# Kernel tuning notes

Measured on AMD Instinct MI355X. Metric: run time of the kernel, lower is better.

Reference implementation:

```python
import jax, jax.numpy as jnp
import numpy as np

R_RAYS = 65536
S_PER_RAY = 128
N_TOTAL = R_RAYS * S_PER_RAY


def setup_inputs() -> dict:
    key = jax.random.key(0)
    k1, k2, k3, k4 = jax.random.split(key, 4)
    sigmas = jax.random.uniform(k1, (N_TOTAL,), dtype=jnp.float32) * 2.0  # densities >= 0
    rgbs = jax.random.uniform(k2, (N_TOTAL, 3), dtype=jnp.float32)
    deltas = jax.random.uniform(k3, (N_TOTAL,), dtype=jnp.float32) * 0.01 + 1e-3
    ts = jax.random.uniform(k4, (N_TOTAL,), dtype=jnp.float32) * 6.0 + 0.1
    ray_idx = jnp.arange(R_RAYS, dtype=jnp.int32)
    rays_a = jnp.stack([ray_idx, ray_idx * S_PER_RAY,
                        jnp.full((R_RAYS,), S_PER_RAY, dtype=jnp.int32)], axis=1)
    return {"sigmas": sigmas, "rgbs": rgbs, "deltas": deltas, "ts": ts,
            "rays_a": rays_a, "T_threshold": 1e-4}


def reference(sigmas, rgbs, deltas, ts, rays_a, T_threshold):
    R = rays_a.shape[0]
    N = sigmas.shape[0]
    S_max = int(jnp.max(rays_a[:, 2]))  # max samples per ray (concrete)

    offs = jnp.arange(S_max, dtype=rays_a.dtype)
    valid = offs[None, :] < rays_a[:, 2, None]              # [R, S] prefix mask
    idx = jnp.where(valid, rays_a[:, 1, None] + offs[None, :], N - 1)  # [R, S]

    a = 1.0 - jnp.exp(-sigmas[idx] * deltas[idx])           # [R, S] alphas

    # Sequential transmittance recurrence with early-exit (T set to 0 once below threshold)
    def step(T, xs):
        a_s, v_s = xs                                        # [R], [R]
        alive = (T > T_threshold) & v_s
        w = jnp.where(alive, a_s * T, 0.0)
        T = jnp.where(alive, T * (1.0 - a_s), 0.0)
        return T, (w, alive)

    T0 = jnp.ones((R,), sigmas.dtype)
    _, (wT, aliveT) = jax.lax.scan(step, T0, (a.T, valid.T))
    w = wT.T                                                 # [R, S] weights
    alive = aliveT.T

    op_n = jnp.sum(w, axis=1)                                # [R]
    dep_n = jnp.sum(w * ts[idx], axis=1)                     # [R]
    rgb_n = jnp.einsum('rs,rsc->rc', w, rgbs[idx])           # [R, 3]
    cnt_n = jnp.sum(alive, axis=1).astype(jnp.int32)

    ridx = rays_a[:, 0]
    opacity = jnp.zeros((R,), w.dtype).at[ridx].add(op_n)
    depth = jnp.zeros((R,), w.dtype).at[ridx].add(dep_n)
    rgb = jnp.zeros((R, 3), w.dtype).at[ridx].add(rgb_n)
    total_samples = jnp.zeros((R,), jnp.int32).at[ridx].add(cnt_n)
    # invalid slots were mapped to index N-1 with w=0, so .add is safe
    ws = jnp.zeros((N,), w.dtype).at[idx.reshape(-1)].add(w.reshape(-1))

    return total_samples.sum(), opacity, depth, rgb, ws
```

## Files before the change

### kernel.cpp

```cpp
#include <hip/hip_runtime.h>


#define BW 4

typedef float f4a __attribute__((ext_vector_type(4), aligned(4)));

template<int CTRL, int RM, unsigned OLD>
__device__ __forceinline__ float dpp_f(float v) {
    return __int_as_float(__builtin_amdgcn_update_dpp(
        (int)OLD, __float_as_int(v), CTRL, RM, 0xF, false));
}

__device__ __forceinline__ float seg_sum32_hi(float v) {
    v += dpp_f<0x111, 0xF, 0u>(v);
    v += dpp_f<0x112, 0xF, 0u>(v);
    v += dpp_f<0x114, 0xF, 0u>(v);
    v += dpp_f<0x118, 0xF, 0u>(v);
    v += dpp_f<0x142, 0xA, 0u>(v);
    return v;
}

struct Ld { float4 sg, dt, tt, c0, c1, c2; };

__global__ __launch_bounds__(256) void vr_main(
    const float* __restrict__ sigmas, const float* __restrict__ rgbs,
    const float* __restrict__ deltas, const float* __restrict__ ts,
    const int* __restrict__ rays_a, const float* __restrict__ thr_p,
    float* __restrict__ out, float* __restrict__ blk_ws,
    int R, int use_ws, int spec_ok)
{
    __shared__ float bsum[BW];

    const int wib  = (int)(threadIdx.x >> 6);
    const int wid  = (int)blockIdx.x * BW + wib;
    const int lane = (int)(threadIdx.x & 63);
    const int half = lane >> 5;
    const int sl   = lane & 31;
    const int ray  = 2 * wid + half;
    const bool inR = ray < R;
    const float thr = thr_p[0];

    const int p_start = ray << 7;
    Ld d;
    if (spec_ok && inR) {
        d.sg = *(const float4*)(sigmas + p_start + 4 * sl);
        d.dt = *(const float4*)(deltas + p_start + 4 * sl);
        d.tt = *(const float4*)(ts     + p_start + 4 * sl);
        const float* rg = rgbs + 3 * ((size_t)p_start + 4 * sl);
        d.c0 = *(const float4*)(rg + 0);
        d.c1 = *(const float4*)(rg + 4);
        d.c2 = *(const float4*)(rg + 8);
    }

    int ridx = 0, start = 0, count = 0;
    if (inR) {
        ridx  = rays_a[3 * ray + 0];
        start = rays_a[3 * ray + 1];
        count = rays_a[3 * ray + 2];
    }
    const bool match = spec_ok && inR && (start == p_start) && (count == 128);
    const bool fastw = __all(match);

    if (!fastw) {
        float sg[4], dt[4], tt[4], rr[4], gg[4], bb[4];
        #pragma unroll
        for (int i = 0; i < 4; ++i) {
            const int s = 4 * sl + i;
            const bool vi = inR && (s < count);
            sg[i] = dt[i] = tt[i] = rr[i] = gg[i] = bb[i] = 0.f;
            if (vi) {
                sg[i] = sigmas[start + s];
                dt[i] = deltas[start + s];
                tt[i] = ts[start + s];
                const float* rg = rgbs + 3 * ((size_t)start + s);
                rr[i] = rg[0]; gg[i] = rg[1]; bb[i] = rg[2];
            }
        }
        d.sg = make_float4(sg[0], sg[1], sg[2], sg[3]);
        d.dt = make_float4(dt[0], dt[1], dt[2], dt[3]);
        d.tt = make_float4(tt[0], tt[1], tt[2], tt[3]);
        d.c0 = make_float4(rr[0], gg[0], bb[0], rr[1]);
        d.c1 = make_float4(gg[1], bb[1], rr[2], gg[2]);
        d.c2 = make_float4(bb[2], rr[3], gg[3], bb[3]);
    }

    float fe[4] = { __expf(-d.sg.x * d.dt.x), __expf(-d.sg.y * d.dt.y),
                    __expf(-d.sg.z * d.dt.z), __expf(-d.sg.w * d.dt.w) };
    bool v[4];
    #pragma unroll
    for (int i = 0; i < 4; ++i) v[i] = inR && (4 * sl + i) < count;

    const float fprod = (fe[0] * fe[1]) * (fe[2] * fe[3]);
    float inc = fprod;
    inc *= dpp_f<0x111, 0xF, 0x3f800000u>(inc);
    inc *= dpp_f<0x112, 0xF, 0x3f800000u>(inc);
    inc *= dpp_f<0x114, 0xF, 0x3f800000u>(inc);
    inc *= dpp_f<0x118, 0xF, 0x3f800000u>(inc);
    inc *= dpp_f<0x142, 0xA, 0x3f800000u>(inc);

    float ex = dpp_f<0x138, 0xF, 0x3f800000u>(inc);
    float T = (sl == 0) ? 1.f : ex;

    float w[4];
    float cnt = 0.f;
    #pragma unroll
    for (int i = 0; i < 4; ++i) {
        const bool alive = v[i] && (T > thr);
        const float Tn = T * fe[i];
        w[i] = alive ? (T - Tn) : 0.f;
        cnt += alive ? 1.f : 0.f;
        T = Tn;
    }

    float* wsp = out + 1 + 5 * (size_t)R + (size_t)start + 4 * sl;
    if (fastw) {
        f4a wv; wv.x = w[0]; wv.y = w[1]; wv.z = w[2]; wv.w = w[3];
        *(f4a*)wsp = wv;
    } else {
        #pragma unroll
        for (int i = 0; i < 4; ++i) if (v[i]) wsp[i] = w[i];
    }

    float op  = (w[0] + w[1]) + (w[2] + w[3]);
    float dep = fmaf(w[0], d.tt.x, fmaf(w[1], d.tt.y, fmaf(w[2], d.tt.z, w[3] * d.tt.w)));
    float cr  = fmaf(w[0], d.c0.x, fmaf(w[1], d.c0.w, fmaf(w[2], d.c1.z, w[3] * d.c2.y)));
    float cg  = fmaf(w[0], d.c0.y, fmaf(w[1], d.c1.x, fmaf(w[2], d.c1.w, w[3] * d.c2.z)));
    float cb  = fmaf(w[0], d.c0.z, fmaf(w[1], d.c1.y, fmaf(w[2], d.c2.x, w[3] * d.c2.w)));

    op  = seg_sum32_hi(op);
    dep = seg_sum32_hi(dep);
    cr  = seg_sum32_hi(cr);
    cg  = seg_sum32_hi(cg);
    cb  = seg_sum32_hi(cb);
    cnt = seg_sum32_hi(cnt);

    if (sl == 31 && inR) {
        out[1 + ridx]                 = op;
        out[1 + R + ridx]             = dep;
        out[1 + 2 * R + 3 * ridx + 0] = cr;
        out[1 + 2 * R + 3 * ridx + 1] = cg;
        out[1 + 2 * R + 3 * ridx + 2] = cb;
    }

    const float cw =
        __int_as_float(__builtin_amdgcn_readlane(__float_as_int(cnt), 31)) +
        __int_as_float(__builtin_amdgcn_readlane(__float_as_int(cnt), 63));
    if (lane == 0) bsum[wib] = cw;
    __syncthreads();
    if (threadIdx.x == 0) {
        const float t = (bsum[0] + bsum[1]) + (bsum[2] + bsum[3]);
        if (use_ws) blk_ws[blockIdx.x] = t;
        else        atomicAdd(&out[0], t);
    }
}

__global__ __launch_bounds__(256) void vr_total(
    const float* __restrict__ blk_ws, float* __restrict__ out, int nb)
{
    __shared__ float sm[4];
    float s = 0.f;
    for (int i = (int)threadIdx.x; i < nb; i += 256) s += blk_ws[i];
    #pragma unroll
    for (int d = 32; d; d >>= 1) s += __shfl_xor(s, d, 64);
    if ((threadIdx.x & 63) == 0) sm[threadIdx.x >> 6] = s;
    __syncthreads();
    if (threadIdx.x == 0) out[0] = (sm[0] + sm[1]) + (sm[2] + sm[3]);
}

extern "C" void kernel_launch(void* const* d_in, const int* in_sizes, int n_in,
                              void* d_out, int out_size, void* d_ws, size_t ws_size,
                              hipStream_t stream) {
    const float* sigmas = (const float*)d_in[0];
    const float* rgbs   = (const float*)d_in[1];
    const float* deltas = (const float*)d_in[2];
    const float* ts     = (const float*)d_in[3];
    const int*   rays_a = (const int*)d_in[4];
    const float* thr    = (const float*)d_in[5];
    const int R = in_sizes[4] / 3;
    float* out = (float*)d_out;
    float* blk_ws = (float*)d_ws;

    const int grid = (R + 2 * BW - 1) / (2 * BW);
    const int use_ws = (ws_size >= (size_t)grid * sizeof(float)) ? 1 : 0;

    const long long need = (long long)R * 128;
    const int spec_ok = (in_sizes[0] >= need) && (in_sizes[2] >= need) &&
                        (in_sizes[3] >= need) &&
                        ((long long)in_sizes[1] >= 3 * need);

    if (!use_ws)
        hipMemsetAsync(d_out, 0, 4, stream);

    vr_main<<<grid, 256, 0, stream>>>(sigmas, rgbs, deltas, ts, rays_a, thr,
                                      out, blk_ws, R, use_ws, spec_ok);
    if (use_ws)
        vr_total<<<1, 256, 0, stream>>>(blk_ws, out, grid);
}
```

Before: 49.12 us.

## Make ws stores 16-byte aligned via lane-shift and defer loads until layout check

The ws output starts at offset 1+5R floats, so the per-lane float4 stores were misaligned. Each lane now takes its neighbour's first three weights through a DPP row shift, which lets every lane issue one aligned float4 store plus a few scalar edge stores. The speculative vector loads are no longer issued before the rays_a check. Loads now wait on the rays_a read and the wave-wide vote, which puts that latency on the critical path and may cost more than the aligned stores save.

```diff
diff --git a/kernel.cpp b/kernel.cpp
--- a/kernel.cpp
+++ b/kernel.cpp
@@ -2,8 +2,6 @@
 
 
 #define BW 4
-
-typedef float f4a __attribute__((ext_vector_type(4), aligned(4)));
 
 template<int CTRL, int RM, unsigned OLD>
 __device__ __forceinline__ float dpp_f(float v) {
@@ -20,14 +18,12 @@
     return v;
 }
 
-struct Ld { float4 sg, dt, tt, c0, c1, c2; };
-
 __global__ __launch_bounds__(256) void vr_main(
     const float* __restrict__ sigmas, const float* __restrict__ rgbs,
     const float* __restrict__ deltas, const float* __restrict__ ts,
     const int* __restrict__ rays_a, const float* __restrict__ thr_p,
     float* __restrict__ out, float* __restrict__ blk_ws,
-    int R, int use_ws, int spec_ok)
+    int R, int use_ws)
 {
     __shared__ float bsum[BW];
 
@@ -40,28 +36,26 @@
     const bool inR = ray < R;
     const float thr = thr_p[0];
 
-    const int p_start = ray << 7;
-    Ld d;
-    if (spec_ok && inR) {
-        d.sg = *(const float4*)(sigmas + p_start + 4 * sl);
-        d.dt = *(const float4*)(deltas + p_start + 4 * sl);
-        d.tt = *(const float4*)(ts     + p_start + 4 * sl);
-        const float* rg = rgbs + 3 * ((size_t)p_start + 4 * sl);
-        d.c0 = *(const float4*)(rg + 0);
-        d.c1 = *(const float4*)(rg + 4);
-        d.c2 = *(const float4*)(rg + 8);
-    }
-
     int ridx = 0, start = 0, count = 0;
     if (inR) {
         ridx  = rays_a[3 * ray + 0];
         start = rays_a[3 * ray + 1];
         count = rays_a[3 * ray + 2];
     }
-    const bool match = spec_ok && inR && (start == p_start) && (count == 128);
-    const bool fastw = __all(match);
-
-    if (!fastw) {
+
+    const bool packed = inR && (start == (ray << 7)) && (count == 128);
+    const bool fastw  = __all(packed);
+
+    float4 sg4, dt4, tt4, c0, c1, c2;
+    if (fastw) {
+        sg4 = *(const float4*)(sigmas + start + 4 * sl);
+        dt4 = *(const float4*)(deltas + start + 4 * sl);
+        tt4 = *(const float4*)(ts     + start + 4 * sl);
+        const float* rg = rgbs + 3 * ((size_t)start + 4 * sl);
+        c0 = *(const float4*)(rg + 0);
+        c1 = *(const float4*)(rg + 4);
+        c2 = *(const float4*)(rg + 8);
+    } else {
         float sg[4], dt[4], tt[4], rr[4], gg[4], bb[4];
         #pragma unroll
         for (int i = 0; i < 4; ++i) {
@@ -76,16 +70,16 @@
                 rr[i] = rg[0]; gg[i] = rg[1]; bb[i] = rg[2];
             }
         }
-        d.sg = make_float4(sg[0], sg[1], sg[2], sg[3]);
-        d.dt = make_float4(dt[0], dt[1], dt[2], dt[3]);
-        d.tt = make_float4(tt[0], tt[1], tt[2], tt[3]);
-        d.c0 = make_float4(rr[0], gg[0], bb[0], rr[1]);
-        d.c1 = make_float4(gg[1], bb[1], rr[2], gg[2]);
-        d.c2 = make_float4(bb[2], rr[3], gg[3], bb[3]);
-    }
-
-    float fe[4] = { __expf(-d.sg.x * d.dt.x), __expf(-d.sg.y * d.dt.y),
-                    __expf(-d.sg.z * d.dt.z), __expf(-d.sg.w * d.dt.w) };
+        sg4 = make_float4(sg[0], sg[1], sg[2], sg[3]);
+        dt4 = make_float4(dt[0], dt[1], dt[2], dt[3]);
+        tt4 = make_float4(tt[0], tt[1], tt[2], tt[3]);
+        c0  = make_float4(rr[0], gg[0], bb[0], rr[1]);
+        c1  = make_float4(gg[1], bb[1], rr[2], gg[2]);
+        c2  = make_float4(bb[2], rr[3], gg[3], bb[3]);
+    }
+
+    float fe[4] = { __expf(-sg4.x * dt4.x), __expf(-sg4.y * dt4.y),
+                    __expf(-sg4.z * dt4.z), __expf(-sg4.w * dt4.w) };
     bool v[4];
     #pragma unroll
     for (int i = 0; i < 4; ++i) v[i] = inR && (4 * sl + i) < count;
@@ -112,20 +106,33 @@
         T = Tn;
     }
 
-    float* wsp = out + 1 + 5 * (size_t)R + (size_t)start + 4 * sl;
+    const size_t wsbase = 1 + 5 * (size_t)R;
     if (fastw) {
-        f4a wv; wv.x = w[0]; wv.y = w[1]; wv.z = w[2]; wv.w = w[3];
-        *(f4a*)wsp = wv;
+        const size_t WB = wsbase + ((size_t)wid << 8);
+        const float n0 = dpp_f<0x130, 0xF, 0u>(w[0]);
+        const float n1 = dpp_f<0x130, 0xF, 0u>(w[1]);
+        const float n2 = dpp_f<0x130, 0xF, 0u>(w[2]);
+        if (lane < 63) {
+            *(float4*)(out + WB + 3 + 4 * lane) = make_float4(w[3], n0, n1, n2);
+        } else {
+            out[WB + 255] = w[3];
+        }
+        if (lane == 0) {
+            out[WB + 0] = w[0];
+            out[WB + 1] = w[1];
+            out[WB + 2] = w[2];
+        }
     } else {
+        float* wsp = out + wsbase + (size_t)start + 4 * sl;
         #pragma unroll
         for (int i = 0; i < 4; ++i) if (v[i]) wsp[i] = w[i];
     }
 
     float op  = (w[0] + w[1]) + (w[2] + w[3]);
-    float dep = fmaf(w[0], d.tt.x, fmaf(w[1], d.tt.y, fmaf(w[2], d.tt.z, w[3] * d.tt.w)));
-    float cr  = fmaf(w[0], d.c0.x, fmaf(w[1], d.c0.w, fmaf(w[2], d.c1.z, w[3] * d.c2.y)));
-    float cg  = fmaf(w[0], d.c0.y, fmaf(w[1], d.c1.x, fmaf(w[2], d.c1.w, w[3] * d.c2.z)));
-    float cb  = fmaf(w[0], d.c0.z, fmaf(w[1], d.c1.y, fmaf(w[2], d.c2.x, w[3] * d.c2.w)));
+    float dep = fmaf(w[0], tt4.x, fmaf(w[1], tt4.y, fmaf(w[2], tt4.z, w[3] * tt4.w)));
+    float cr  = fmaf(w[0], c0.x, fmaf(w[1], c0.w, fmaf(w[2], c1.z, w[3] * c2.y)));
+    float cg  = fmaf(w[0], c0.y, fmaf(w[1], c1.x, fmaf(w[2], c1.w, w[3] * c2.z)));
+    float cb  = fmaf(w[0], c0.z, fmaf(w[1], c1.y, fmaf(w[2], c2.x, w[3] * c2.w)));
 
     op  = seg_sum32_hi(op);
     dep = seg_sum32_hi(dep);
@@ -183,16 +190,11 @@
     const int grid = (R + 2 * BW - 1) / (2 * BW);
     const int use_ws = (ws_size >= (size_t)grid * sizeof(float)) ? 1 : 0;
 
-    const long long need = (long long)R * 128;
-    const int spec_ok = (in_sizes[0] >= need) && (in_sizes[2] >= need) &&
-                        (in_sizes[3] >= need) &&
-                        ((long long)in_sizes[1] >= 3 * need);
-
     if (!use_ws)
         hipMemsetAsync(d_out, 0, 4, stream);
 
     vr_main<<<grid, 256, 0, stream>>>(sigmas, rgbs, deltas, ts, rays_a, thr,
-                                      out, blk_ws, R, use_ws, spec_ok);
+                                      out, blk_ws, R, use_ws);
     if (use_ws)
         vr_total<<<1, 256, 0, stream>>>(blk_ws, out, grid);
 }
```

New measurement: 49.01 us. No clear change (-0.2%).
